# Kernel optimization log

Measured on AMD Instinct MI355X. Metric: run time of the kernel, lower is better.

Reference implementation:

```python
import math
import jax, jax.numpy as jnp
import numpy as np

D_MODEL = 1024
N_HEADS = 16
HEAD_DIM = D_MODEL // N_HEADS
B, L = 1, 4096


def _slopes(n_heads):
    ratio = 2.0 ** (-8.0 / n_heads)
    return jnp.asarray([ratio ** (i + 1) for i in range(n_heads)], dtype=jnp.float32)


def setup_inputs() -> dict:
    key = jax.random.key(0)
    ks = jax.random.split(key, 5)
    scale = 1.0 / math.sqrt(D_MODEL)
    return {
        "x": jax.random.normal(ks[0], (B, L, D_MODEL), dtype=jnp.float32),
        "q_w": jax.random.normal(ks[1], (D_MODEL, D_MODEL), dtype=jnp.float32) * scale,
        "k_w": jax.random.normal(ks[2], (D_MODEL, D_MODEL), dtype=jnp.float32) * scale,
        "v_w": jax.random.normal(ks[3], (D_MODEL, D_MODEL), dtype=jnp.float32) * scale,
        "o_w": jax.random.normal(ks[4], (D_MODEL, D_MODEL), dtype=jnp.float32) * scale,
    }


def reference(x, q_w, k_w, v_w, o_w):
    b, l, _ = x.shape
    # projections -> [B, H, L, hd]
    def proj(w):
        return (x @ w).reshape(b, l, N_HEADS, HEAD_DIM).transpose(0, 2, 1, 3)
    q, k, v = proj(q_w), proj(k_w), proj(v_w)

    scale = math.sqrt(HEAD_DIM)
    scores = jnp.einsum("bhid,bhjd->bhij", q, k) / scale  # [B,H,L,L]

    pos = jnp.arange(l)
    distance = jnp.abs(pos[None, :] - pos[:, None]).astype(jnp.float32)  # [L,L]
    alibi = -distance[None, :, :] * _slopes(N_HEADS)[:, None, None]       # [H,L,L]
    scores = scores + alibi[None]

    causal = pos[None, :] <= pos[:, None]  # j <= i
    scores = jnp.where(causal[None, None], scores, -jnp.inf)

    attn = jax.nn.softmax(scores, axis=-1)
    out = jnp.einsum("bhij,bhjd->bhid", attn, v)
    out = out.transpose(0, 2, 1, 3).reshape(b, l, D_MODEL)
    return out @ o_w
```

## Files before the change

kernel.cpp:

```cpp
#include <hip/hip_runtime.h>

#define L_SEQ 4096
#define DM    1024
#define NH    16
#define HD    64

typedef unsigned short ushort_t;
typedef __attribute__((ext_vector_type(8))) short bf16x8;
typedef __attribute__((ext_vector_type(4))) float f32x4;

__device__ inline unsigned short f2bf(float f) {
    union { float f; unsigned int u; } v; v.f = f;
    unsigned int r = v.u + 0x7fffu + ((v.u >> 16) & 1u);
    return (unsigned short)(r >> 16);
}

__device__ inline unsigned cvt_pk_bf16(float lo, float hi) {
    unsigned w;
    asm("v_cvt_pk_bf16_f32 %0, %1, %2" : "=v"(w) : "v"(lo), "v"(hi));
    return w;
}

__device__ inline float ex2(float x) {
#if __has_builtin(__builtin_amdgcn_exp2f)
    return __builtin_amdgcn_exp2f(x);
#else
    return exp2f(x);
#endif
}

__device__ inline void load_lds16(const ushort_t* g, ushort_t* l) {
    __builtin_amdgcn_global_load_lds(
        (const __attribute__((address_space(1))) unsigned int*)g,
        (__attribute__((address_space(3))) unsigned int*)l, 16, 0, 0);
}

__device__ inline bool detect_f32(const ushort_t* xraw) {
    __shared__ int s_flag;
    const int t = threadIdx.x;
    if (t < 64) {
        unsigned e = (xraw[2 * t] >> 7) & 0xFFu;
        unsigned long long m = __ballot(e >= 0x88u);
        if (t == 0) s_flag = (__popcll(m) >= 8) ? 1 : 0;
    }
    __syncthreads();
    return s_flag != 0;
}

__global__ __launch_bounds__(256) void convert_all(const void* __restrict__ xv,
                                                   const void* __restrict__ w0,
                                                   const void* __restrict__ w1,
                                                   const void* __restrict__ w2,
                                                   const void* __restrict__ w3,
                                                   ushort_t* __restrict__ xb,
                                                   ushort_t* __restrict__ wT) {
    bool f32 = detect_f32((const ushort_t*)xv);
    const int z = blockIdx.z;
    const int t = threadIdx.x;

    if (z == 4) {
        const int B0 = (blockIdx.y * 16 + blockIdx.x) * 16384;
        #pragma unroll
        for (int it = 0; it < 8; ++it) {
            const int i = B0 + it * 2048 + t * 8;
            if (f32) {
                const float* xf = (const float*)xv;
                float4 v0 = *(const float4*)(xf + i);
                float4 v1 = *(const float4*)(xf + i + 4);
                uint4 u;
                u.x = cvt_pk_bf16(v0.x, v0.y);
                u.y = cvt_pk_bf16(v0.z, v0.w);
                u.z = cvt_pk_bf16(v1.x, v1.y);
                u.w = cvt_pk_bf16(v1.z, v1.w);
                *(uint4*)(xb + i) = u;
            } else {
                *(uint4*)(xb + i) = *(const uint4*)((const ushort_t*)xv + i);
            }
        }
        return;
    }

    const void* w = (z == 0) ? w0 : (z == 1) ? w1 : (z == 2) ? w2 : w3;
    ushort_t* out = wT + (size_t)z * (DM * DM);
    __shared__ ushort_t T[64][65];
    const int k0 = blockIdx.x * 64, n0 = blockIdx.y * 64;
    #pragma unroll
    for (int i = 0; i < 16; ++i) {
        int e = t + i * 256;
        int r = e >> 6, c = e & 63;
        T[r][c] = f32 ? f2bf(((const float*)w)[(size_t)(k0 + r) * DM + n0 + c])
                      : ((const ushort_t*)w)[(size_t)(k0 + r) * DM + n0 + c];
    }
    __syncthreads();
    #pragma unroll
    for (int i = 0; i < 16; ++i) {
        int e = t + i * 256;
        int d = e >> 6, l = e & 63;
        out[(size_t)(n0 + d) * DM + k0 + l] = T[l][d];
    }
}

__device__ inline void gemm128_body(const ushort_t* __restrict__ A,
                                    const ushort_t* __restrict__ Bt,
                                    void* __restrict__ Cv, int cmode,
                                    int m0, int n0) {
    constexpr int K = 1024, NOUT = 1024;
    __shared__ ushort_t As[128 * 64];
    __shared__ ushort_t Bs[128 * 64];

    const int t = threadIdx.x, lane = t & 63, wave = t >> 6;
    const int l15 = lane & 15, quad = lane >> 4;
    const int mw = (wave >> 1) * 64, nw = (wave & 1) * 64;
    const int srow = lane >> 3;
    const int sgr  = (lane & 7) ^ (lane >> 3);
    const int swz  = l15 & 7;

    f32x4 acc[4][4] = {};

    for (int k0 = 0; k0 < K; k0 += 64) {
        #pragma unroll
        for (int i = 0; i < 4; ++i) {
            const int j = wave * 4 + i;
            load_lds16(A  + (size_t)(m0 + 8 * j + srow) * K + k0 + sgr * 8,
                       &As[8 * j * 64]);
            load_lds16(Bt + (size_t)(n0 + 8 * j + srow) * K + k0 + sgr * 8,
                       &Bs[8 * j * 64]);
        }
        __syncthreads();

        #pragma unroll
        for (int kt = 0; kt < 2; ++kt) {
            bf16x8 af[4], bf[4];
            #pragma unroll
            for (int i = 0; i < 4; ++i) {
                af[i] = *(const bf16x8*)&As[(mw + i * 16 + l15) * 64
                                            + (((kt * 4 + quad) ^ swz) * 8)];
                bf[i] = *(const bf16x8*)&Bs[(nw + i * 16 + l15) * 64
                                            + (((kt * 4 + quad) ^ swz) * 8)];
            }
            #pragma unroll
            for (int mt = 0; mt < 4; ++mt)
                #pragma unroll
                for (int nt = 0; nt < 4; ++nt)
                    acc[mt][nt] = __builtin_amdgcn_mfma_f32_16x16x32_bf16(
                        af[mt], bf[nt], acc[mt][nt], 0, 0, 0);
        }
        __syncthreads();
    }

    if (cmode == 2) {
        ushort_t* Vt = (ushort_t*)Cv;
        #pragma unroll
        for (int mt = 0; mt < 4; ++mt)
            #pragma unroll
            for (int nt = 0; nt < 4; ++nt) {
                int col  = n0 + nw + nt * 16 + l15;
                int row0 = m0 + mw + mt * 16 + quad * 4;
                ushort_t pk[4] = {f2bf(acc[mt][nt][0]), f2bf(acc[mt][nt][1]),
                                  f2bf(acc[mt][nt][2]), f2bf(acc[mt][nt][3])};
                *(uint2*)&Vt[(size_t)col * L_SEQ + row0] = *(const uint2*)pk;
            }
        return;
    }

    const int odd = lane & 1;
    #pragma unroll
    for (int mtp = 0; mtp < 2; ++mtp)
        #pragma unroll
        for (int nt = 0; nt < 4; ++nt)
            #pragma unroll
            for (int r = 0; r < 4; ++r) {
                float zA = acc[2 * mtp][nt][r];
                float zB = acc[2 * mtp + 1][nt][r];
                float send = odd ? zA : zB;
                float got  = __shfl_xor(send, 1);
                const int row = m0 + mw + (2 * mtp + odd) * 16 + quad * 4 + r;
                const int col = n0 + nw + nt * 16 + (l15 & ~1);
                if (cmode == 1) {
                    float2 w2 = odd ? make_float2(got, zB) : make_float2(zA, got);
                    *(float2*)((float*)Cv + (size_t)row * NOUT + col) = w2;
                } else {
                    float lo = odd ? got : zA;
                    float hi = odd ? zB  : got;
                    unsigned w = cvt_pk_bf16(lo, hi);
                    *(unsigned*)((ushort_t*)Cv + (size_t)row * NOUT + col) = w;
                }
            }
}

__global__ __launch_bounds__(256) void qkv128(const ushort_t* __restrict__ xb,
                                              const ushort_t* __restrict__ wT,
                                              ushort_t* Qp, ushort_t* Kp, ushort_t* Vt) {
    const int b = blockIdx.x;
    const int n0 = (b & 7) * 128;
    const int u  = b >> 3;
    const int m0 = (u / 3) * 128;
    const int z  = u % 3;
    const ushort_t* Bt = wT + (size_t)z * (DM * DM);
    if (z == 0)      gemm128_body(xb, Bt, Qp, 0, m0, n0);
    else if (z == 1) gemm128_body(xb, Bt, Kp, 0, m0, n0);
    else             gemm128_body(xb, Bt, Vt, 2, m0, n0);
}

__global__ __launch_bounds__(256) void ogemm128(const void* __restrict__ xdet,
                                                const ushort_t* __restrict__ An,
                                                const ushort_t* __restrict__ woT,
                                                void* __restrict__ C) {
    bool f32 = detect_f32((const ushort_t*)xdet);
    const int b = blockIdx.x;
    const int n0 = (b & 7) * 128, m0 = (b >> 3) * 128;
    gemm128_body(An, woT, C, f32 ? 1 : 0, m0, n0);
}

__global__ __launch_bounds__(512) void attn_kernel(const ushort_t* __restrict__ Q,
                                                   const ushort_t* __restrict__ Kp,
                                                   const ushort_t* __restrict__ Vt,
                                                   ushort_t* __restrict__ O) {
    __shared__ ushort_t Ks[2][128 * 64];
    __shared__ ushort_t Vs[2][64 * 128];
    __shared__ ushort_t Pt[128 * 128];

    const int b    = blockIdx.x;
    const int h    = 2 * (b & 7) + ((b >> 3) & 1);
    const int px   = b >> 4;
    const int t    = threadIdx.x;
    const int lane = t & 63, wave = t >> 6;
    const int l15  = lane & 15, quad = lane >> 4;
    const float LOG2E  = 1.44269504f;
    const float slope2 = exp2f(-0.5f * (float)(h + 1)) * LOG2E;
    const float c0     = 0.125f * LOG2E;
    const float qd4f   = (float)(quad * 4);

    const int krow = lane >> 3, kgr = (lane & 7) ^ (lane >> 3);
    const int vsub = lane >> 4;
    const int swz = l15 & 7;

    auto stage_load = [&](int buf, int kv0) {
        #pragma unroll
        for (int i = 0; i < 2; ++i) {
            const int j = wave * 2 + i;
            load_lds16(Kp + (size_t)(kv0 + 8 * j + krow) * DM + h * HD + kgr * 8,
                       &Ks[buf][8 * j * 64]);
        }
        #pragma unroll
        for (int i = 0; i < 2; ++i) {
            const int j = wave * 2 + i;
            const int d = 4 * j + vsub;
            const int g = (lane & 15) ^ (4 * (j & 1) + vsub);
            load_lds16(Vt + (size_t)(h * HD + d) * L_SEQ + kv0 + g * 8,
                       &Vs[buf][4 * j * 128]);
        }
    };

    int par = 0;
    stage_load(0, 0);

    #pragma unroll
    for (int half = 0; half < 2; ++half) {
        const int qb = half ? px : (31 - px);
        const int q0 = qb * 128;
        const int qg = q0 + wave * 16 + l15;
        const float qf = (float)qg;
        const int nst = half ? (px + 1) : (32 - px);

        bf16x8 bq[2];
        #pragma unroll
        for (int kt = 0; kt < 2; ++kt)
            bq[kt] = *(const bf16x8*)(Q + (size_t)qg * DM + h * HD + kt * 32 + quad * 8);

        f32x4 acc_o[4] = {};
        float l_r = 0.f;

        for (int s = 0; s < nst; ++s) {
            const int kv0 = s * 128;
            __syncthreads();

            const int nkv0 = (s + 1 < nst) ? (s + 1) * 128 : 0;
            stage_load(par ^ 1, nkv0);

            f32x4 sacc[8];
            #pragma unroll
            for (int mt = 0; mt < 8; ++mt) sacc[mt] = (f32x4){0.f, 0.f, 0.f, 0.f};
            __builtin_amdgcn_s_setprio(1);
            #pragma unroll
            for (int kt = 0; kt < 2; ++kt)
                #pragma unroll
                for (int mt = 0; mt < 8; ++mt) {
                    bf16x8 a = *(const bf16x8*)&Ks[par][(mt * 16 + l15) * 64
                                                        + (((kt * 4 + quad) ^ swz) * 8)];
                    sacc[mt] = __builtin_amdgcn_mfma_f32_16x16x32_bf16(a, bq[kt], sacc[mt], 0, 0, 0);
                }
            __builtin_amdgcn_s_setprio(0);

            const bool diag = (kv0 + 128 > q0);
            const float off = slope2 * ((float)kv0 + qd4f - qf);
            float rs = 0.f;
            #pragma unroll
            for (int mt = 0; mt < 8; ++mt)
                #pragma unroll
                for (int r = 0; r < 4; ++r) {
                    float kvl = (float)(mt * 16 + r);
                    float s2  = fmaf(sacc[mt][r], c0, fmaf(slope2, kvl, off));
                    if (diag) {
                        int kvg = kv0 + mt * 16 + quad * 4 + r;
                        s2 = (kvg <= qg) ? s2 : -1e30f;
                    }
                    float p = ex2(s2);
                    sacc[mt][r] = p;
                    rs += p;
                }
            rs += __shfl_xor(rs, 16);
            rs += __shfl_xor(rs, 32);
            l_r += rs;

            #pragma unroll
            for (int mt = 0; mt < 8; ++mt) {
                union { float f; unsigned u; } a0, a1, a2, a3;
                a0.f = sacc[mt][0]; a1.f = sacc[mt][1];
                a2.f = sacc[mt][2]; a3.f = sacc[mt][3];
                uint2 w;
                w.x = __builtin_amdgcn_perm(a1.u, a0.u, 0x07060302);
                w.y = __builtin_amdgcn_perm(a3.u, a2.u, 0x07060302);
                const int g = mt * 2 + (quad >> 1);
                *(uint2*)&Pt[(wave * 16 + l15) * 128
                             + ((g ^ swz) * 8 + (quad & 1) * 4)] = w;
            }
            __threadfence_block();

            __builtin_amdgcn_s_setprio(1);
            #pragma unroll
            for (int kt = 0; kt < 4; ++kt) {
                bf16x8 a = *(const bf16x8*)&Pt[(wave * 16 + l15) * 128
                                               + (((kt * 4 + quad) ^ swz) * 8)];
                #pragma unroll
                for (int nt = 0; nt < 4; ++nt) {
                    bf16x8 bvv = *(const bf16x8*)&Vs[par][(nt * 16 + l15) * 128
                                                          + (((kt * 4 + quad) ^ swz) * 8)];
                    acc_o[nt] = __builtin_amdgcn_mfma_f32_16x16x32_bf16(a, bvv, acc_o[nt], 0, 0, 0);
                }
            }
            __builtin_amdgcn_s_setprio(0);

            par ^= 1;
        }

        float linv[4];
        #pragma unroll
        for (int r = 0; r < 4; ++r) linv[r] = 1.0f / __shfl(l_r, quad * 4 + r);
        #pragma unroll
        for (int nt = 0; nt < 4; ++nt)
            #pragma unroll
            for (int r = 0; r < 4; ++r) {
                int row = q0 + wave * 16 + quad * 4 + r;
                O[(size_t)row * DM + h * HD + nt * 16 + l15] = f2bf(acc_o[nt][r] * linv[r]);
            }
    }
}

__global__ __launch_bounds__(512, 4) void attn_split(const ushort_t* __restrict__ Q,
                                                     const ushort_t* __restrict__ Kp,
                                                     const ushort_t* __restrict__ Vt,
                                                     float* __restrict__ Op,
                                                     float* __restrict__ Lp) {
    __shared__ ushort_t Ks[128 * 64];
    __shared__ ushort_t Vs[64 * 128];
    __shared__ ushort_t Pt[128 * 128];

    const int b    = blockIdx.x;
    const int bb   = b & 255;
    const int v    = b >> 8;
    const int h    = 2 * (bb & 7) + ((bb >> 3) & 1);
    const int px   = bb >> 4;
    const int t    = threadIdx.x;
    const int lane = t & 63, wave = t >> 6;
    const int l15  = lane & 15, quad = lane >> 4;
    const float LOG2E  = 1.44269504f;
    const float slope2 = exp2f(-0.5f * (float)(h + 1)) * LOG2E;
    const float c0     = 0.125f * LOG2E;
    const float qd4f   = (float)(quad * 4);

    const int krow = lane >> 3, kgr = (lane & 7) ^ (lane >> 3);
    const int vsub = lane >> 4;
    const int swz = l15 & 7;

    float* Opv = Op + (size_t)v * L_SEQ * DM;

    auto stage_load = [&](int kv0) {
        #pragma unroll
        for (int i = 0; i < 2; ++i) {
            const int j = wave * 2 + i;
            load_lds16(Kp + (size_t)(kv0 + 8 * j + krow) * DM + h * HD + kgr * 8,
                       &Ks[8 * j * 64]);
        }
        #pragma unroll
        for (int i = 0; i < 2; ++i) {
            const int j = wave * 2 + i;
            const int d = 4 * j + vsub;
            const int g = (lane & 15) ^ (4 * (j & 1) + vsub);
            load_lds16(Vt + (size_t)(h * HD + d) * L_SEQ + kv0 + g * 8,
                       &Vs[4 * j * 128]);
        }
    };

    #pragma unroll
    for (int half = 0; half < 2; ++half) {
        const int qb = half ? px : (31 - px);
        const int q0 = qb * 128;
        const int qg = q0 + wave * 16 + l15;
        const float qf = (float)qg;
        const int nst = half ? (px + 1) : (32 - px);

        bf16x8 bq[2];
        #pragma unroll
        for (int kt = 0; kt < 2; ++kt)
            bq[kt] = *(const bf16x8*)(Q + (size_t)qg * DM + h * HD + kt * 32 + quad * 8);

        f32x4 acc_o[4] = {};
        float l_r = 0.f;

        for (int s = v; s < nst; s += 2) {
            const int kv0 = s * 128;
            stage_load(kv0);
            __syncthreads();

            f32x4 sacc[8];
            #pragma unroll
            for (int mt = 0; mt < 8; ++mt) sacc[mt] = (f32x4){0.f, 0.f, 0.f, 0.f};
            __builtin_amdgcn_s_setprio(1);
            #pragma unroll
            for (int kt = 0; kt < 2; ++kt)
                #pragma unroll
                for (int mt = 0; mt < 8; ++mt) {
                    bf16x8 a = *(const bf16x8*)&Ks[(mt * 16 + l15) * 64
                                                   + (((kt * 4 + quad) ^ swz) * 8)];
                    sacc[mt] = __builtin_amdgcn_mfma_f32_16x16x32_bf16(a, bq[kt], sacc[mt], 0, 0, 0);
                }
            __builtin_amdgcn_s_setprio(0);

            const bool diag = (kv0 + 128 > q0);
            const float off = slope2 * ((float)kv0 + qd4f - qf);
            float rs = 0.f;
            #pragma unroll
            for (int mt = 0; mt < 8; ++mt)
                #pragma unroll
                for (int r = 0; r < 4; ++r) {
                    float kvl = (float)(mt * 16 + r);
                    float s2  = fmaf(sacc[mt][r], c0, fmaf(slope2, kvl, off));
                    if (diag) {
                        int kvg = kv0 + mt * 16 + quad * 4 + r;
                        s2 = (kvg <= qg) ? s2 : -1e30f;
                    }
                    float p = ex2(s2);
                    sacc[mt][r] = p;
                    rs += p;
                }
            rs += __shfl_xor(rs, 16);
            rs += __shfl_xor(rs, 32);
            l_r += rs;

            #pragma unroll
            for (int mt = 0; mt < 8; ++mt) {
                union { float f; unsigned u; } a0, a1, a2, a3;
                a0.f = sacc[mt][0]; a1.f = sacc[mt][1];
                a2.f = sacc[mt][2]; a3.f = sacc[mt][3];
                uint2 w;
                w.x = __builtin_amdgcn_perm(a1.u, a0.u, 0x07060302);
                w.y = __builtin_amdgcn_perm(a3.u, a2.u, 0x07060302);
                const int g = mt * 2 + (quad >> 1);
                *(uint2*)&Pt[(wave * 16 + l15) * 128
                             + ((g ^ swz) * 8 + (quad & 1) * 4)] = w;
            }
            __threadfence_block();

            __builtin_amdgcn_s_setprio(1);
            #pragma unroll
            for (int kt = 0; kt < 4; ++kt) {
                bf16x8 a = *(const bf16x8*)&Pt[(wave * 16 + l15) * 128
                                               + (((kt * 4 + quad) ^ swz) * 8)];
                #pragma unroll
                for (int nt = 0; nt < 4; ++nt) {
                    bf16x8 bvv = *(const bf16x8*)&Vs[(nt * 16 + l15) * 128
                                                     + (((kt * 4 + quad) ^ swz) * 8)];
                    acc_o[nt] = __builtin_amdgcn_mfma_f32_16x16x32_bf16(a, bvv, acc_o[nt], 0, 0, 0);
                }
            }
            __builtin_amdgcn_s_setprio(0);

            __syncthreads();
        }

        #pragma unroll
        for (int nt = 0; nt < 4; ++nt)
            #pragma unroll
            for (int r = 0; r < 4; ++r) {
                int row = q0 + wave * 16 + quad * 4 + r;
                Opv[(size_t)row * DM + h * HD + nt * 16 + l15] = acc_o[nt][r];
            }
        if (quad == 0)
            Lp[(size_t)v * (NH * L_SEQ) + (size_t)h * L_SEQ + qg] = l_r;
    }
}

__global__ __launch_bounds__(256) void attn_combine(const float* __restrict__ Op,
                                                    const float* __restrict__ Lp,
                                                    ushort_t* __restrict__ An) {
    const int i = (blockIdx.x * 256 + threadIdx.x) * 8;
    const int row = i >> 10;
    const int h   = (i & 1023) >> 6;
    const float l0 = Lp[(size_t)h * L_SEQ + row];
    const float l1 = Lp[(size_t)NH * L_SEQ + (size_t)h * L_SEQ + row];
    const float linv = 1.0f / (l0 + l1);
    const size_t V1 = (size_t)L_SEQ * DM;
    float4 a0 = *(const float4*)(Op + i);
    float4 a1 = *(const float4*)(Op + i + 4);
    float4 b0 = *(const float4*)(Op + V1 + i);
    float4 b1 = *(const float4*)(Op + V1 + i + 4);
    uint4 u;
    u.x = cvt_pk_bf16((a0.x + b0.x) * linv, (a0.y + b0.y) * linv);
    u.y = cvt_pk_bf16((a0.z + b0.z) * linv, (a0.w + b0.w) * linv);
    u.z = cvt_pk_bf16((a1.x + b1.x) * linv, (a1.y + b1.y) * linv);
    u.w = cvt_pk_bf16((a1.z + b1.z) * linv, (a1.w + b1.w) * linv);
    *(uint4*)(An + i) = u;
}

extern "C" void kernel_launch(void* const* d_in, const int* in_sizes, int n_in,
                              void* d_out, int out_size, void* d_ws, size_t ws_size,
                              hipStream_t stream) {
    const void* x  = d_in[0];
    const void* wq = d_in[1];
    const void* wk = d_in[2];
    const void* wv = d_in[3];
    const void* wo = d_in[4];

    const size_t SZ = (size_t)L_SEQ * DM;
    const size_t WZ = (size_t)DM * DM;
    ushort_t* xb = (ushort_t*)d_ws;
    ushort_t* wT = xb + SZ;
    ushort_t* Qp = wT + 4 * WZ;
    ushort_t* Kp = Qp + SZ;
    ushort_t* Vt = Kp + SZ;
    ushort_t* An = xb;

    float* Op = (float*)(Vt + SZ);
    float* Lp = Op + 2 * SZ;
    const size_t need = 40ull * 1024 * 1024 + 2 * SZ * 4 + 2ull * NH * L_SEQ * 4;

    convert_all<<<dim3(16, 16, 5), 256, 0, stream>>>(x, wq, wk, wv, wo, xb, wT);
    qkv128<<<768, 256, 0, stream>>>(xb, wT, Qp, Kp, Vt);
    if (ws_size >= need) {
        attn_split<<<512, 512, 0, stream>>>(Qp, Kp, Vt, Op, Lp);
        attn_combine<<<2048, 256, 0, stream>>>(Op, Lp, An);
    } else {
        attn_kernel<<<256, 512, 0, stream>>>(Qp, Kp, Vt, An);
    }
    ogemm128<<<256, 256, 0, stream>>>(x, An, wT + 3 * WZ, d_out);
}
```

Baseline: 221.7 us.

## Split attention KV loop four ways across blocks with a four-way combine

Result: slower. 260.9 us (+17.7%).

```diff
diff --git a/kernel.cpp b/kernel.cpp
--- a/kernel.cpp
+++ b/kernel.cpp
@@ -523,6 +523,167 @@
     *(uint4*)(An + i) = u;
 }
 
+__global__ __launch_bounds__(512, 8) void attn_split4(const ushort_t* __restrict__ Q,
+                                                      const ushort_t* __restrict__ Kp,
+                                                      const ushort_t* __restrict__ Vt,
+                                                      float* __restrict__ Op,
+                                                      float* __restrict__ Lp) {
+    __shared__ ushort_t Ks[64 * 64];
+    __shared__ ushort_t Vs[64 * 64];
+    __shared__ ushort_t Pt[128 * 64];
+
+    const int b    = blockIdx.x;
+    const int bb   = b & 255;
+    const int v    = b >> 8;
+    const int h    = 2 * (bb & 7) + ((bb >> 3) & 1);
+    const int px   = bb >> 4;
+    const int t    = threadIdx.x;
+    const int lane = t & 63, wave = t >> 6;
+    const int l15  = lane & 15, quad = lane >> 4;
+    const float LOG2E  = 1.44269504f;
+    const float slope2 = exp2f(-0.5f * (float)(h + 1)) * LOG2E;
+    const float c0     = 0.125f * LOG2E;
+    const float qd4f   = (float)(quad * 4);
+
+    const int krow = lane >> 3, kgr = (lane & 7) ^ (lane >> 3);
+    const int swz = l15 & 7;
+
+    float* Opv = Op + (size_t)v * L_SEQ * DM;
+
+    auto stage_load = [&](int kv0) {
+        load_lds16(Kp + (size_t)(kv0 + 8 * wave + krow) * DM + h * HD + kgr * 8,
+                   &Ks[8 * wave * 64]);
+        load_lds16(Vt + (size_t)(h * HD + 8 * wave + krow) * L_SEQ + kv0 + kgr * 8,
+                   &Vs[8 * wave * 64]);
+    };
+
+    #pragma unroll
+    for (int half = 0; half < 2; ++half) {
+        const int qb = half ? px : (31 - px);
+        const int q0 = qb * 128;
+        const int qg = q0 + wave * 16 + l15;
+        const float qf = (float)qg;
+        const int nst = half ? (2 * px + 2) : (64 - 2 * px);
+
+        bf16x8 bq[2];
+        #pragma unroll
+        for (int kt = 0; kt < 2; ++kt)
+            bq[kt] = *(const bf16x8*)(Q + (size_t)qg * DM + h * HD + kt * 32 + quad * 8);
+
+        f32x4 acc_o[4] = {};
+        float l_r = 0.f;
+
+        for (int s = v; s < nst; s += 4) {
+            const int kv0 = s * 64;
+            stage_load(kv0);
+            __syncthreads();
+
+            f32x4 sacc[4];
+            #pragma unroll
+            for (int mt = 0; mt < 4; ++mt) sacc[mt] = (f32x4){0.f, 0.f, 0.f, 0.f};
+            __builtin_amdgcn_s_setprio(1);
+            #pragma unroll
+            for (int kt = 0; kt < 2; ++kt)
+                #pragma unroll
+                for (int mt = 0; mt < 4; ++mt) {
+                    bf16x8 a = *(const bf16x8*)&Ks[(mt * 16 + l15) * 64
+                                                   + (((kt * 4 + quad) ^ swz) * 8)];
+                    sacc[mt] = __builtin_amdgcn_mfma_f32_16x16x32_bf16(a, bq[kt], sacc[mt], 0, 0, 0);
+                }
+            __builtin_amdgcn_s_setprio(0);
+
+            const bool diag = (kv0 + 64 > q0);
+            const float off = slope2 * ((float)kv0 + qd4f - qf);
+            float rs = 0.f;
+            #pragma unroll
+            for (int mt = 0; mt < 4; ++mt)
+                #pragma unroll
+                for (int r = 0; r < 4; ++r) {
+                    float kvl = (float)(mt * 16 + r);
+                    float s2  = fmaf(sacc[mt][r], c0, fmaf(slope2, kvl, off));
+                    if (diag) {
+                        int kvg = kv0 + mt * 16 + quad * 4 + r;
+                        s2 = (kvg <= qg) ? s2 : -1e30f;
+                    }
+                    float p = ex2(s2);
+                    sacc[mt][r] = p;
+                    rs += p;
+                }
+            rs += __shfl_xor(rs, 16);
+            rs += __shfl_xor(rs, 32);
+            l_r += rs;
+
+            #pragma unroll
+            for (int mt = 0; mt < 4; ++mt) {
+                union { float f; unsigned u; } a0, a1, a2, a3;
+                a0.f = sacc[mt][0]; a1.f = sacc[mt][1];
+                a2.f = sacc[mt][2]; a3.f = sacc[mt][3];
+                uint2 w;
+                w.x = __builtin_amdgcn_perm(a1.u, a0.u, 0x07060302);
+                w.y = __builtin_amdgcn_perm(a3.u, a2.u, 0x07060302);
+                const int g = mt * 2 + (quad >> 1);
+                *(uint2*)&Pt[(wave * 16 + l15) * 64
+                             + ((g ^ swz) * 8 + (quad & 1) * 4)] = w;
+            }
+            __threadfence_block();
+
+            __builtin_amdgcn_s_setprio(1);
+            #pragma unroll
+            for (int kt = 0; kt < 2; ++kt) {
+                bf16x8 a = *(const bf16x8*)&Pt[(wave * 16 + l15) * 64
+                                               + (((kt * 4 + quad) ^ swz) * 8)];
+                #pragma unroll
+                for (int nt = 0; nt < 4; ++nt) {
+                    bf16x8 bvv = *(const bf16x8*)&Vs[(nt * 16 + l15) * 64
+                                                     + (((kt * 4 + quad) ^ swz) * 8)];
+                    acc_o[nt] = __builtin_amdgcn_mfma_f32_16x16x32_bf16(a, bvv, acc_o[nt], 0, 0, 0);
+                }
+            }
+            __builtin_amdgcn_s_setprio(0);
+
+            __syncthreads();
+        }
+
+        #pragma unroll
+        for (int nt = 0; nt < 4; ++nt)
+            #pragma unroll
+            for (int r = 0; r < 4; ++r) {
+                int row = q0 + wave * 16 + quad * 4 + r;
+                Opv[(size_t)row * DM + h * HD + nt * 16 + l15] = acc_o[nt][r];
+            }
+        if (quad == 0)
+            Lp[(size_t)v * (NH * L_SEQ) + (size_t)h * L_SEQ + qg] = l_r;
+    }
+}
+
+__global__ __launch_bounds__(256) void attn_combine4(const float* __restrict__ Op,
+                                                     const float* __restrict__ Lp,
+                                                     ushort_t* __restrict__ An) {
+    const int i = (blockIdx.x * 256 + threadIdx.x) * 8;
+    const int row = i >> 10;
+    const int h   = (i & 1023) >> 6;
+    float l = 0.f;
+    #pragma unroll
+    for (int v = 0; v < 4; ++v)
+        l += Lp[(size_t)v * (NH * L_SEQ) + (size_t)h * L_SEQ + row];
+    const float linv = 1.0f / l;
+    const size_t V1 = (size_t)L_SEQ * DM;
+    float4 s0 = {0, 0, 0, 0}, s1 = {0, 0, 0, 0};
+    #pragma unroll
+    for (int v = 0; v < 4; ++v) {
+        float4 a0 = *(const float4*)(Op + (size_t)v * V1 + i);
+        float4 a1 = *(const float4*)(Op + (size_t)v * V1 + i + 4);
+        s0.x += a0.x; s0.y += a0.y; s0.z += a0.z; s0.w += a0.w;
+        s1.x += a1.x; s1.y += a1.y; s1.z += a1.z; s1.w += a1.w;
+    }
+    uint4 u;
+    u.x = cvt_pk_bf16(s0.x * linv, s0.y * linv);
+    u.y = cvt_pk_bf16(s0.z * linv, s0.w * linv);
+    u.z = cvt_pk_bf16(s1.x * linv, s1.y * linv);
+    u.w = cvt_pk_bf16(s1.z * linv, s1.w * linv);
+    *(uint4*)(An + i) = u;
+}
+
 extern "C" void kernel_launch(void* const* d_in, const int* in_sizes, int n_in,
                               void* d_out, int out_size, void* d_ws, size_t ws_size,
                               hipStream_t stream) {
@@ -542,14 +703,20 @@
     ushort_t* An = xb;
 
     float* Op = (float*)(Vt + SZ);
-    float* Lp = Op + 2 * SZ;
-    const size_t need = 40ull * 1024 * 1024 + 2 * SZ * 4 + 2ull * NH * L_SEQ * 4;
+    float* Lp4 = Op + 4 * SZ;
+    float* Lp2 = Op + 2 * SZ;
+    const size_t base  = 40ull * 1024 * 1024;
+    const size_t need4 = base + 4 * SZ * 4 + 4ull * NH * L_SEQ * 4;
+    const size_t need2 = base + 2 * SZ * 4 + 2ull * NH * L_SEQ * 4;
 
     convert_all<<<dim3(16, 16, 5), 256, 0, stream>>>(x, wq, wk, wv, wo, xb, wT);
     qkv128<<<768, 256, 0, stream>>>(xb, wT, Qp, Kp, Vt);
-    if (ws_size >= need) {
-        attn_split<<<512, 512, 0, stream>>>(Qp, Kp, Vt, Op, Lp);
-        attn_combine<<<2048, 256, 0, stream>>>(Op, Lp, An);
+    if (ws_size >= need4) {
+        attn_split4<<<1024, 512, 0, stream>>>(Qp, Kp, Vt, Op, Lp4);
+        attn_combine4<<<2048, 256, 0, stream>>>(Op, Lp4, An);
+    } else if (ws_size >= need2) {
+        attn_split<<<512, 512, 0, stream>>>(Qp, Kp, Vt, Op, Lp2);
+        attn_combine<<<2048, 256, 0, stream>>>(Op, Lp2, An);
     } else {
         attn_kernel<<<256, 512, 0, stream>>>(Qp, Kp, Vt, An);
     }
```
